# Kernel optimization log

Hardware: AMD Instinct MI355X
Metric: run time of the kernel (lower is better)

## Reference

```python
import jax, jax.numpy as jnp
import numpy as np

Na, Np, F, C, H, L, OUT = 50000, 100000, 128, 128, 8, 2, 64
D = C // H  # head dim = 16
E = 150000


def setup_inputs() -> dict:
    key = jax.random.key(0)
    ks = jax.random.split(key, 16)
    p = lambda k, shape: jax.random.normal(k, shape, jnp.float32) * 0.05
    return {
        "x_author": jax.random.normal(ks[0], (Na, F), jnp.float32),
        "x_paper": jax.random.normal(ks[1], (Np, F), jnp.float32),
        # per-node-type input projections (HGT.lin_dict)
        "win_w": p(ks[2], (2, F, C)), "win_b": p(ks[3], (2, C)),
        # per-layer, per-node-type K/Q/V linears of HGTConv
        "kqv_w": p(ks[4], (L, 2, 3, C, C)), "kqv_b": p(ks[5], (L, 2, 3, C)),
        # per-layer, per-node-type output linear a_lin
        "a_w": p(ks[6], (L, 2, C, C)), "a_b": p(ks[7], (L, 2, C)),
        # per-layer, per-node-type skip gate (init 1 like PyG)
        "skip": jnp.ones((L, 2), jnp.float32),
        # per-layer, per-edge-type relation matrices a_rel/m_rel and prior p_rel
        "rel_a": p(ks[8], (L, 2, H, D, D)), "rel_m": p(ks[9], (L, 2, H, D, D)),
        "rel_p": jnp.ones((L, 2, H), jnp.float32),
        # final classifier on author nodes
        "out_w": p(ks[10], (C, OUT)), "out_b": p(ks[11], (OUT,)),
        # edge type 0: author -> paper ('writes'); edge type 1: paper -> author (reverse)
        "ei_writes_src": jax.random.randint(ks[12], (E,), 0, Na, jnp.int32),
        "ei_writes_dst": jax.random.randint(ks[13], (E,), 0, Np, jnp.int32),
        "ei_rev_src": jax.random.randint(ks[14], (E,), 0, Np, jnp.int32),
        "ei_rev_dst": jax.random.randint(ks[15], (E,), 0, Na, jnp.int32),
    }


def _segment_softmax(alpha, dst, n):
    # softmax of alpha [E, H] over edges grouped by destination node (PyG softmax)
    m = jnp.full((n, alpha.shape[1]), -jnp.inf, alpha.dtype).at[dst].max(alpha)
    ex = jnp.exp(alpha - m[dst])
    s = jnp.zeros((n, alpha.shape[1]), alpha.dtype).at[dst].add(ex)
    return ex / (s[dst] + 1e-16)


def _hgt_forward(x_author, x_paper, win_w, win_b, kqv_w, kqv_b, a_w, a_b,
                 skip, rel_a, rel_m, rel_p, out_w, out_b, ei):
    # per-node-type input linear + relu
    xs = [jax.nn.relu(x_author @ win_w[0] + win_b[0]),
          jax.nn.relu(x_paper @ win_w[1] + win_b[1])]
    edge_types = [(0, 1, ei[0], ei[1]),  # author -> paper
                  (1, 0, ei[2], ei[3])]  # paper -> author
    nl = kqv_w.shape[0]
    inv_sqrt_d = np.float32(1.0 / np.sqrt(D))
    for l in range(nl):
        # K/Q/V per node type, shape [N_t, H, D]
        kqv = [[(xs[t] @ kqv_w[l, t, i] + kqv_b[l, t, i]).reshape(-1, H, D)
                for i in range(3)] for t in range(2)]
        agg = [jnp.zeros((xs[t].shape[0], H, D), xs[t].dtype) for t in range(2)]
        for e, (st, dt, src, dst) in enumerate(edge_types):
            # relation-specific transforms at node level, then gather at edges
            kn = jnp.einsum('nhd,hde->nhe', kqv[st][0], rel_a[l, e])
            vn = jnp.einsum('nhd,hde->nhe', kqv[st][2], rel_m[l, e])
            alpha = jnp.einsum('ehd,ehd->eh', kqv[dt][1][dst], kn[src])
            alpha = alpha * rel_p[l, e] * inv_sqrt_d
            alpha = _segment_softmax(alpha, dst, xs[dt].shape[0])
            agg[dt] = agg[dt].at[dst].add(alpha[:, :, None] * vn[src])
        new_xs = []
        for t in range(2):
            o = jax.nn.gelu(agg[t].reshape(-1, C), approximate=False)
            o = o @ a_w[l, t] + a_b[l, t]
            g = jax.nn.sigmoid(skip[l, t])
            new_xs.append(g * o + (1.0 - g) * xs[t])  # skip connection (dims match)
        xs = new_xs
    return xs[0] @ out_w + out_b  # author output


def reference(x_author, x_paper, win_w, win_b, kqv_w, kqv_b, a_w, a_b, skip,
              rel_a, rel_m, rel_p, out_w, out_b,
              ei_writes_src, ei_writes_dst, ei_rev_src, ei_rev_dst):
    ei = (ei_writes_src, ei_writes_dst, ei_rev_src, ei_rev_dst)
    return _hgt_forward(x_author, x_paper, win_w, win_b, kqv_w, kqv_b,
                        a_w, a_b, skip, rel_a, rel_m, rel_p, out_w, out_b, ei)
```

## Files before the change

kernel.cpp:

```cpp
#include <hip/hip_runtime.h>
#include <math.h>

namespace {

constexpr int Na = 50000, Np = 100000, L = 2, E = 150000;
constexpr int SCAN_TILE = 2048;

typedef __attribute__((ext_vector_type(8))) short short8v;
typedef __attribute__((ext_vector_type(4))) float f32x4;

__device__ inline float geluf(float x){ return 0.5f*x*(1.0f + erff(x*0.7071067811865476f)); }

__device__ inline float bf2f(unsigned short u){ return __uint_as_float(((unsigned)u) << 16); }
__device__ inline unsigned short f2bf(float f){
  unsigned u = __float_as_uint(f);
  u += 0x7FFFu + ((u >> 16) & 1u);
  return (unsigned short)(u >> 16);
}
__device__ inline unsigned pk2(float a, float b){
  return (unsigned)f2bf(a) | ((unsigned)f2bf(b) << 16);
}

struct StF32 {
  using T = float;
  static __device__ short8v ld8(const T* __restrict__ p){
    float4 lo = *reinterpret_cast<const float4*>(p);
    float4 hi = *reinterpret_cast<const float4*>(p+4);
    short8v v;
    v[0]=(short)f2bf(lo.x); v[1]=(short)f2bf(lo.y); v[2]=(short)f2bf(lo.z); v[3]=(short)f2bf(lo.w);
    v[4]=(short)f2bf(hi.x); v[5]=(short)f2bf(hi.y); v[6]=(short)f2bf(hi.z); v[7]=(short)f2bf(hi.w);
    return v;
  }
};
struct StBF16 {
  using T = unsigned short;
  static __device__ short8v ld8(const T* __restrict__ p){
    return *reinterpret_cast<const short8v*>(p);
  }
  static __device__ void ld16(const T* __restrict__ p, float* o){
    const uint4* q = reinterpret_cast<const uint4*>(p);
    #pragma unroll
    for (int half = 0; half < 2; ++half){
      uint4 u = q[half];
      o[half*8+0] = bf2f((unsigned short)(u.x & 0xffff));
      o[half*8+1] = bf2f((unsigned short)(u.x >> 16));
      o[half*8+2] = bf2f((unsigned short)(u.y & 0xffff));
      o[half*8+3] = bf2f((unsigned short)(u.y >> 16));
      o[half*8+4] = bf2f((unsigned short)(u.z & 0xffff));
      o[half*8+5] = bf2f((unsigned short)(u.z >> 16));
      o[half*8+6] = bf2f((unsigned short)(u.w & 0xffff));
      o[half*8+7] = bf2f((unsigned short)(u.w >> 16));
    }
  }
};

__global__ void zero_int_kernel(int* __restrict__ p, int n){
  int i = blockIdx.x*256 + threadIdx.x;
  int stride = gridDim.x*256;
  for (; i < n; i += stride) p[i] = 0;
}

__global__ void diag_kernel(float* o, float v){
  if (threadIdx.x == 0 && blockIdx.x == 0) o[0] = v;
}

__global__ void hist_kernel(const int* __restrict__ dst, int* __restrict__ counts, int nE){
  int e = blockIdx.x*256 + threadIdx.x;
  if (e >= nE) return;
  atomicAdd(&counts[dst[e]], 1);
}

__global__ void scan_a(const int* __restrict__ counts, int* __restrict__ bsum, int n){
  int base = blockIdx.x*SCAN_TILE;
  int s = 0;
  for (int i = threadIdx.x; i < SCAN_TILE; i += 256){
    int g = base + i;
    s += (g < n) ? counts[g] : 0;
  }
  __shared__ int red[256];
  red[threadIdx.x] = s;
  __syncthreads();
  for (int off = 128; off > 0; off >>= 1){
    if (threadIdx.x < off) red[threadIdx.x] += red[threadIdx.x + off];
    __syncthreads();
  }
  if (threadIdx.x == 0) bsum[blockIdx.x] = red[0];
}

__global__ void scan_b(int* __restrict__ bsum, int nb){
  __shared__ int sh[1024];
  int t = threadIdx.x;
  int v = (t < nb) ? bsum[t] : 0;
  sh[t] = v;
  __syncthreads();
  for (int off = 1; off < 1024; off <<= 1){
    int add = (t >= off) ? sh[t-off] : 0;
    __syncthreads();
    sh[t] += add;
    __syncthreads();
  }
  if (t < nb) bsum[t] = sh[t] - v;
}

__global__ void scan_c(int* __restrict__ counts, const int* __restrict__ bsum,
                       int* __restrict__ rp, int n){
  int base = blockIdx.x*SCAN_TILE;
  __shared__ int sh[SCAN_TILE];
  for (int i = threadIdx.x; i < SCAN_TILE; i += 256){
    int g = base + i;
    sh[i] = (g < n) ? counts[g] : 0;
  }
  __syncthreads();
  int t = threadIdx.x;
  int loc[8], s = 0;
  #pragma unroll
  for (int i = 0; i < 8; ++i){ loc[i] = s; s += sh[t*8 + i]; }
  __shared__ int red[256];
  red[t] = s;
  __syncthreads();
  for (int off = 1; off < 256; off <<= 1){
    int add = (t >= off) ? red[t-off] : 0;
    __syncthreads();
    red[t] += add;
    __syncthreads();
  }
  int texcl = red[t] - s + bsum[blockIdx.x];
  #pragma unroll
  for (int i = 0; i < 8; ++i){
    int g = base + t*8 + i;
    if (g < n){
      int v = texcl + loc[i];
      rp[g] = v;
      counts[g] = v;
      if (g == n-1) rp[n] = v + sh[t*8 + i];
    }
  }
}

__global__ void fill_slots_kernel(const int* __restrict__ src, const int* __restrict__ dst,
                                  int* __restrict__ cursor, int* __restrict__ slots, int nE){
  int e = blockIdx.x*256 + threadIdx.x;
  if (e >= nE) return;
  int slot = atomicAdd(&cursor[dst[e]], 1);
  slots[slot] = src[e];
}

__global__ void eff_w_kernel(const float* __restrict__ kqv_w, const float* __restrict__ kqv_b,
                             const float* __restrict__ rel_a, const float* __restrict__ rel_m,
                             float* __restrict__ effw, float* __restrict__ effb){
  int idx = blockIdx.x*256 + threadIdx.x;
  if (idx >= 2*2*2*128*128) return;
  int j = idx & 127; int f = (idx >> 7) & 127; int c = idx >> 14;
  int kv = c & 1, t = (c >> 1) & 1, l = c >> 2;
  int h = j >> 4, e2 = j & 15;
  int i = (kv == 0) ? 0 : 2;
  const float* W = kqv_w + ((size_t)(((l*2 + t)*3 + i)*128) + f)*128 + h*16;
  const float* A = ((kv == 0) ? rel_a : rel_m) + ((size_t)(l*2 + t)*8 + h)*256;
  float acc = 0.f;
  #pragma unroll
  for (int d = 0; d < 16; ++d) acc += W[d]*A[d*16 + e2];
  effw[(size_t)c*16384 + f*128 + j] = acc;
  if (f == 0){
    const float* B = kqv_b + (size_t)((l*2 + t)*3 + i)*128 + h*16;
    float ab = 0.f;
    #pragma unroll
    for (int d = 0; d < 16; ++d) ab += B[d]*A[d*16 + e2];
    effb[c*128 + j] = ab;
  }
}

struct PrepSrc { const float* s[19]; };
__global__ void prep_w_kernel(PrepSrc P, unsigned short* __restrict__ wbf){
  int idx = blockIdx.x*256 + threadIdx.x;
  if (idx >= 19*16384) return;
  int s = idx >> 14, j = idx & 16383;
  int n = j >> 7, k = j & 127;
  int nc = (s == 18) ? 64 : 128;
  if (n >= nc) return;
  wbf[(size_t)s*16384 + n*128 + k] = f2bf(P.s[s][(size_t)k*nc + n]);
}

__device__ inline void stage_w(short* Bs, const unsigned short* __restrict__ WT, int t, int rows){
  for (int c = t; c < rows*16; c += 512){
    int r = c >> 4, c16 = c & 15;
    short8v v = *reinterpret_cast<const short8v*>(&WT[r*128 + c16*8]);
    *reinterpret_cast<short8v*>(&Bs[r*128 + ((c16 ^ (r&7))<<3)]) = v;
  }
}

struct GemmArgs {
  const void* X[2];
  const unsigned short* WT[2];
  const float* bias[2];
  void* Y[2];
  const unsigned short* skip_x[2];
  const float* skip_s[2];
  int N[2];
  int blocks0;
};

template<int BN, int GELU_IN, int RELU_OUT, int SKIP, typename SIn>
__global__ __launch_bounds__(512) void gemm_kernel(GemmArgs Ar)
{
  __shared__ __align__(16) short As[128*128];
  __shared__ __align__(16) char Braw[32768];
  short* Bs = (short*)Braw;
  const int t = threadIdx.x;
  const int part = (blockIdx.x < Ar.blocks0) ? 0 : 1;
  const int bid = part ? (blockIdx.x - Ar.blocks0) : blockIdx.x;
  const typename SIn::T* X = (const typename SIn::T*)Ar.X[part];
  const unsigned short* WT = Ar.WT[part];
  const float* bias = Ar.bias[part];
  const int N = Ar.N[part];
  const int row0 = bid*128;
  for (int c = t; c < 128*16; c += 512){
    int r = c >> 4, c16 = c & 15;
    int gr = row0 + r;
    short8v v;
    if (gr < N){
      v = SIn::ld8(&X[(size_t)gr*128 + c16*8]);
      if (GELU_IN){
        #pragma unroll
        for (int i = 0; i < 8; ++i){
          float f = geluf(bf2f((unsigned short)v[i]));
          v[i] = (short)f2bf(f);
        }
      }
    } else {
      v = (short8v)0;
    }
    *reinterpret_cast<short8v*>(&As[r*128 + ((c16 ^ (r&7))<<3)]) = v;
  }
  stage_w(Bs, WT, t, BN);
  __syncthreads();
  const int lane = t & 63, wid = t >> 6;
  const int wm = wid >> 2, wn = wid & 3;
  constexpr int NR = BN/64;
  const int lr = lane & 15, lk = lane >> 4;
  f32x4 acc[4][NR] = {};
  #pragma unroll
  for (int kk = 0; kk < 4; ++kk){
    int kc = kk*4 + lk;
    short8v a[4], b[NR];
    #pragma unroll
    for (int m = 0; m < 4; ++m){
      int r = wm*64 + m*16 + lr;
      a[m] = *reinterpret_cast<const short8v*>(&As[r*128 + ((kc ^ (r&7))<<3)]);
    }
    #pragma unroll
    for (int n = 0; n < NR; ++n){
      int col = wn*(BN/4) + n*16 + lr;
      b[n] = *reinterpret_cast<const short8v*>(&Bs[col*128 + ((kc ^ (col&7))<<3)]);
    }
    #pragma unroll
    for (int m = 0; m < 4; ++m)
      #pragma unroll
      for (int n = 0; n < NR; ++n)
        acc[m][n] = __builtin_amdgcn_mfma_f32_16x16x32_bf16(b[n], a[m], acc[m][n], 0, 0, 0);
  }
  __syncthreads();

  if constexpr (BN == 128){
    #pragma unroll
    for (int m = 0; m < 4; ++m){
      int row = wm*64 + m*16 + lr;
      #pragma unroll
      for (int n = 0; n < NR; ++n){
        int col0 = wn*32 + n*16 + lk*4;
        float4 b4 = *reinterpret_cast<const float4*>(&bias[col0]);
        float y0 = acc[m][n][0] + b4.x, y1 = acc[m][n][1] + b4.y;
        float y2 = acc[m][n][2] + b4.z, y3 = acc[m][n][3] + b4.w;
        if (RELU_OUT){
          y0 = fmaxf(y0,0.f); y1 = fmaxf(y1,0.f); y2 = fmaxf(y2,0.f); y3 = fmaxf(y3,0.f);
        }
        uint2 pk; pk.x = pk2(y0,y1); pk.y = pk2(y2,y3);
        int c16 = col0 >> 3;
        *reinterpret_cast<uint2*>(&Bs[row*128 + ((c16 ^ (row&7))<<3) + (col0&7)]) = pk;
      }
    }
    __syncthreads();
    float g = 1.f, og = 0.f;
    if (SKIP){ float sv = *Ar.skip_s[part]; g = 1.f/(1.f + expf(-sv)); og = 1.f - g; }
    unsigned short* out = (unsigned short*)Ar.Y[part];
    const unsigned short* skip_x = Ar.skip_x[part];
    for (int c = t; c < 128*16; c += 512){
      int r = c >> 4, c16 = c & 15;
      int gr = row0 + r;
      if (gr >= N) continue;
      short8v v = *reinterpret_cast<const short8v*>(&Bs[r*128 + ((c16 ^ (r&7))<<3)]);
      if (SKIP){
        short8v s8 = *reinterpret_cast<const short8v*>(&skip_x[(size_t)gr*128 + c16*8]);
        short8v o8;
        #pragma unroll
        for (int i = 0; i < 8; ++i)
          o8[i] = (short)f2bf(g*bf2f((unsigned short)v[i]) + og*bf2f((unsigned short)s8[i]));
        *reinterpret_cast<short8v*>(&out[(size_t)gr*128 + c16*8]) = o8;
      } else {
        *reinterpret_cast<short8v*>(&out[(size_t)gr*128 + c16*8]) = v;
      }
    }
  } else {
    float* Bf = (float*)Braw;
    #pragma unroll
    for (int m = 0; m < 4; ++m){
      int row = wm*64 + m*16 + lr;
      #pragma unroll
      for (int n = 0; n < NR; ++n){
        int col0 = wn*16 + n*16 + lk*4;
        float4 b4 = *reinterpret_cast<const float4*>(&bias[col0]);
        float4 y;
        y.x = acc[m][n][0] + b4.x; y.y = acc[m][n][1] + b4.y;
        y.z = acc[m][n][2] + b4.z; y.w = acc[m][n][3] + b4.w;
        int cf = col0 >> 2;
        *reinterpret_cast<float4*>(&Bf[row*64 + ((cf ^ (row&7))<<2)]) = y;
      }
    }
    __syncthreads();
    float* out = (float*)Ar.Y[part];
    for (int c = t; c < 128*16; c += 512){
      int r = c >> 4, cf = c & 15;
      int gr = row0 + r;
      if (gr >= N) continue;
      float4 v = *reinterpret_cast<const float4*>(&Bf[r*64 + ((cf ^ (r&7))<<2)]);
      *reinterpret_cast<float4*>(&out[(size_t)gr*64 + cf*4]) = v;
    }
  }
}

struct QkvArgs {
  const unsigned short* X[2];
  const unsigned short* WT[2][3];
  const float* bias[2][3];
  unsigned short* out[2][3];
  int N[2];
  int blocks0;
};

__global__ __launch_bounds__(512) void qkv_kernel(QkvArgs Ar)
{
  __shared__ __align__(16) short As[128*128];
  __shared__ __align__(16) short Bs[128*128];
  const int t = threadIdx.x;
  const int part = (blockIdx.x < Ar.blocks0) ? 0 : 1;
  const int bid = part ? (blockIdx.x - Ar.blocks0) : blockIdx.x;
  const unsigned short* X = Ar.X[part];
  const int N = Ar.N[part];
  const int row0 = bid*128;
  for (int c = t; c < 128*16; c += 512){
    int r = c >> 4, c16 = c & 15;
    int gr = row0 + r;
    short8v v = (gr < N) ? *reinterpret_cast<const short8v*>(&X[(size_t)gr*128 + c16*8])
                         : (short8v)0;
    *reinterpret_cast<short8v*>(&As[r*128 + ((c16 ^ (r&7))<<3)]) = v;
  }
  const int lane = t & 63, wid = t >> 6;
  const int wm = wid >> 2, wn = wid & 3;
  const int lr = lane & 15, lk = lane >> 4;
  #pragma unroll
  for (int s = 0; s < 3; ++s){
    __syncthreads();
    stage_w(Bs, Ar.WT[part][s], t, 128);
    __syncthreads();
    f32x4 acc[4][2] = {};
    #pragma unroll
    for (int kk = 0; kk < 4; ++kk){
      int kc = kk*4 + lk;
      short8v a[4], b[2];
      #pragma unroll
      for (int m = 0; m < 4; ++m){
        int r = wm*64 + m*16 + lr;
        a[m] = *reinterpret_cast<const short8v*>(&As[r*128 + ((kc ^ (r&7))<<3)]);
      }
      #pragma unroll
      for (int n = 0; n < 2; ++n){
        int col = wn*32 + n*16 + lr;
        b[n] = *reinterpret_cast<const short8v*>(&Bs[col*128 + ((kc ^ (col&7))<<3)]);
      }
      #pragma unroll
      for (int m = 0; m < 4; ++m)
        #pragma unroll
        for (int n = 0; n < 2; ++n)
          acc[m][n] = __builtin_amdgcn_mfma_f32_16x16x32_bf16(b[n], a[m], acc[m][n], 0, 0, 0);
    }
    __syncthreads();
    const float* bi = Ar.bias[part][s];
    #pragma unroll
    for (int m = 0; m < 4; ++m){
      int row = wm*64 + m*16 + lr;
      #pragma unroll
      for (int n = 0; n < 2; ++n){
        int col0 = wn*32 + n*16 + lk*4;
        float4 b4 = *reinterpret_cast<const float4*>(&bi[col0]);
        uint2 pk;
        pk.x = pk2(acc[m][n][0] + b4.x, acc[m][n][1] + b4.y);
        pk.y = pk2(acc[m][n][2] + b4.z, acc[m][n][3] + b4.w);
        int c16 = col0 >> 3;
        *reinterpret_cast<uint2*>(&Bs[row*128 + ((c16 ^ (row&7))<<3) + (col0&7)]) = pk;
      }
    }
    __syncthreads();
    unsigned short* out = Ar.out[part][s];
    for (int c = t; c < 128*16; c += 512){
      int r = c >> 4, c16 = c & 15;
      int gr = row0 + r;
      if (gr >= N) continue;
      short8v v = *reinterpret_cast<const short8v*>(&Bs[r*128 + ((c16 ^ (r&7))<<3)]);
      *reinterpret_cast<short8v*>(&out[(size_t)gr*128 + c16*8]) = v;
    }
  }
}

struct AttnArgs {
  unsigned short* QA[2];
  const unsigned short* K[2];
  const unsigned short* V[2];
  const int* rp[2];
  const int* slots[2];
  const float* relp[2];
  int N[2];
  int blocks0;
};

__global__ void attn_gather_kernel(AttnArgs Ar){
  const int part = (blockIdx.x < Ar.blocks0) ? 0 : 1;
  const int bid = part ? (blockIdx.x - Ar.blocks0) : blockIdx.x;
  int idx = bid*256 + threadIdx.x;
  const int N = Ar.N[part];
  if (idx >= N*8) return;
  int h = idx & 7, n = idx >> 3;
  unsigned short* QA = Ar.QA[part];
  const unsigned short* K = Ar.K[part];
  const unsigned short* V = Ar.V[part];
  float q[16];
  StBF16::ld16(&QA[(size_t)n*128 + h*16], q);
  float scale_h = Ar.relp[part][h]*0.25f;
  float m = -INFINITY, s = 0.f, acc[16];
  #pragma unroll
  for (int i = 0; i < 16; ++i) acc[i] = 0.f;
  int b = Ar.rp[part][n], e = Ar.rp[part][n+1];
  const int* slots = Ar.slots[part];
  for (int j = b; j < e; ++j){
    int sv = slots[j];
    float kf[16], vf[16];
    StBF16::ld16(&K[(size_t)sv*128 + h*16], kf);
    float a = 0.f;
    #pragma unroll
    for (int i = 0; i < 16; ++i) a += q[i]*kf[i];
    a *= scale_h;
    float mn = fmaxf(m, a);
    float c = expf(m - mn);
    float p = expf(a - mn);
    StBF16::ld16(&V[(size_t)sv*128 + h*16], vf);
    s = s*c + p;
    #pragma unroll
    for (int i = 0; i < 16; ++i) acc[i] = acc[i]*c + p*vf[i];
    m = mn;
  }
  float inv = 1.f/(s + 1e-16f);
  #pragma unroll
  for (int i = 0; i < 16; ++i) QA[(size_t)n*128 + h*16 + i] = f2bf(acc[i]*inv);
}

struct Ptrs {
  const float *x_author, *x_paper, *win_w, *win_b, *kqv_w, *kqv_b, *a_w, *a_b;
  const float *skip, *rel_a, *rel_m, *rel_p, *out_w, *out_b;
  const int *src0, *dst0, *src1, *dst1;
};

static void run_pipeline(const Ptrs& P, float* d_out, char* ws, hipStream_t stream){
  using BF = unsigned short;
  size_t off = 0;
  auto alloc = [&](size_t bytes) -> void* {
    void* p = ws + off;
    off += (bytes + 255) & ~(size_t)255;
    return p;
  };
  BF* X0 = (BF*)alloc((size_t)Na*128*2);
  BF* X1 = (BF*)alloc((size_t)Np*128*2);
  BF* Q0 = (BF*)alloc((size_t)Na*128*2);
  BF* Q1 = (BF*)alloc((size_t)Np*128*2);
  BF* K0 = (BF*)alloc((size_t)Na*128*2);
  BF* K1 = (BF*)alloc((size_t)Np*128*2);
  BF* V0 = (BF*)alloc((size_t)Na*128*2);
  BF* V1 = (BF*)alloc((size_t)Np*128*2);
  float* effw = (float*)alloc((size_t)8*16384*4);
  float* effb = (float*)alloc((size_t)8*128*4);
  BF* wbf = (BF*)alloc((size_t)19*16384*2);
  int* rp0   = (int*)alloc((size_t)(Np+1)*4);
  int* cur0  = (int*)alloc((size_t)Np*4);
  int* slot0 = (int*)alloc((size_t)E*4);
  int* rp1   = (int*)alloc((size_t)(Na+1)*4);
  int* cur1  = (int*)alloc((size_t)Na*4);
  int* slot1 = (int*)alloc((size_t)E*4);
  int* bsum  = (int*)alloc((size_t)1024*4);

  auto cdiv = [](int a, int b){ return (a+b-1)/b; };
  const int geE = cdiv(E, 256);
  const int ga = cdiv(Na, 128), gp = cdiv(Np, 128);
  const int sb0 = cdiv(Np, SCAN_TILE), sb1 = cdiv(Na, SCAN_TILE);

  eff_w_kernel<<<512, 256, 0, stream>>>(P.kqv_w, P.kqv_b, P.rel_a, P.rel_m, effw, effb);

  PrepSrc ps;
  ps.s[0] = P.win_w; ps.s[1] = P.win_w + 16384;
  for (int l = 0; l < 2; ++l)
    for (int t = 0; t < 2; ++t){
      ps.s[2 + l*2 + t]  = P.kqv_w + (size_t)((l*2+t)*3+1)*16384;
      ps.s[6 + l*2 + t]  = effw + (size_t)(l*4+t*2+0)*16384;
      ps.s[10 + l*2 + t] = effw + (size_t)(l*4+t*2+1)*16384;
      ps.s[14 + l*2 + t] = P.a_w + (size_t)(l*2+t)*16384;
    }
  ps.s[18] = P.out_w;
  prep_w_kernel<<<cdiv(19*16384,256),256,0,stream>>>(ps, wbf);

  zero_int_kernel<<<512,256,0,stream>>>(cur0, Np);
  zero_int_kernel<<<512,256,0,stream>>>(cur1, Na);
  hist_kernel<<<geE,256,0,stream>>>(P.dst0, cur0, E);
  hist_kernel<<<geE,256,0,stream>>>(P.dst1, cur1, E);
  scan_a<<<sb0,256,0,stream>>>(cur0, bsum, Np);
  scan_b<<<1,1024,0,stream>>>(bsum, sb0);
  scan_c<<<sb0,256,0,stream>>>(cur0, bsum, rp0, Np);
  scan_a<<<sb1,256,0,stream>>>(cur1, bsum, Na);
  scan_b<<<1,1024,0,stream>>>(bsum, sb1);
  scan_c<<<sb1,256,0,stream>>>(cur1, bsum, rp1, Na);
  fill_slots_kernel<<<geE,256,0,stream>>>(P.src0, P.dst0, cur0, slot0, E);
  fill_slots_kernel<<<geE,256,0,stream>>>(P.src1, P.dst1, cur1, slot1, E);

  auto W = [&](int s){ return wbf + (size_t)s*16384; };

  {
    GemmArgs g{};
    g.X[0] = P.x_author; g.X[1] = P.x_paper;
    g.WT[0] = W(0); g.WT[1] = W(1);
    g.bias[0] = P.win_b; g.bias[1] = P.win_b + 128;
    g.Y[0] = X0; g.Y[1] = X1;
    g.N[0] = Na; g.N[1] = Np; g.blocks0 = ga;
    gemm_kernel<128,0,1,0,StF32><<<ga+gp,512,0,stream>>>(g);
  }

  const int ab0 = cdiv(Np*8,256), ab1 = cdiv(Na*8,256);

  for (int l = 0; l < L; ++l){
    QkvArgs q{};
    q.X[0] = X0; q.X[1] = X1;
    for (int t2 = 0; t2 < 2; ++t2){
      q.WT[t2][0] = W(2+l*2+t2); q.WT[t2][1] = W(6+l*2+t2); q.WT[t2][2] = W(10+l*2+t2);
      q.bias[t2][0] = P.kqv_b + ((l*2+t2)*3+1)*128;
      q.bias[t2][1] = effb + (l*4+t2*2+0)*128;
      q.bias[t2][2] = effb + (l*4+t2*2+1)*128;
    }
    q.out[0][0] = Q0; q.out[0][1] = K0; q.out[0][2] = V0;
    q.out[1][0] = Q1; q.out[1][1] = K1; q.out[1][2] = V1;
    q.N[0] = Na; q.N[1] = Np; q.blocks0 = ga;
    qkv_kernel<<<ga+gp,512,0,stream>>>(q);

    AttnArgs a{};
    a.QA[0] = Q1; a.K[0] = K0; a.V[0] = V0; a.rp[0] = rp0; a.slots[0] = slot0;
    a.relp[0] = P.rel_p + (l*2+0)*8; a.N[0] = Np;
    a.QA[1] = Q0; a.K[1] = K1; a.V[1] = V1; a.rp[1] = rp1; a.slots[1] = slot1;
    a.relp[1] = P.rel_p + (l*2+1)*8; a.N[1] = Na;
    a.blocks0 = ab0;
    attn_gather_kernel<<<ab0+ab1,256,0,stream>>>(a);

    GemmArgs g{};
    g.X[0] = Q0; g.X[1] = Q1;
    g.WT[0] = W(14+l*2+0); g.WT[1] = W(14+l*2+1);
    g.bias[0] = P.a_b + (l*2+0)*128; g.bias[1] = P.a_b + (l*2+1)*128;
    g.Y[0] = X0; g.Y[1] = X1;
    g.skip_x[0] = X0; g.skip_x[1] = X1;
    g.skip_s[0] = P.skip + (l*2+0); g.skip_s[1] = P.skip + (l*2+1);
    g.N[0] = Na; g.N[1] = Np; g.blocks0 = ga;
    gemm_kernel<128,1,0,1,StBF16><<<ga+gp,512,0,stream>>>(g);
  }

  {
    GemmArgs g{};
    g.X[0] = X0; g.X[1] = nullptr;
    g.WT[0] = W(18); g.WT[1] = nullptr;
    g.bias[0] = P.out_b; g.bias[1] = nullptr;
    g.Y[0] = d_out; g.Y[1] = nullptr;
    g.N[0] = Na; g.N[1] = 0; g.blocks0 = ga;
    gemm_kernel<64,0,0,0,StBF16><<<ga,512,0,stream>>>(g);
  }
}

static size_t plan_bytes(){
  auto al = [](size_t x){ return (x + 255) & ~(size_t)255; };
  size_t t = 0;
  t += 4*(al((size_t)Na*128*2) + al((size_t)Np*128*2));
  t += al((size_t)8*16384*4) + al((size_t)8*128*4) + al((size_t)19*16384*2);
  t += al((size_t)(Np+1)*4) + al((size_t)Np*4) + al((size_t)E*4);
  t += al((size_t)(Na+1)*4) + al((size_t)Na*4) + al((size_t)E*4);
  t += al((size_t)1024*4);
  return t;
}

}

extern "C" void kernel_launch(void* const* d_in, const int* in_sizes, int n_in,
                              void* d_out, int out_size, void* d_ws, size_t ws_size,
                              hipStream_t stream){
  Ptrs P;
  P.x_author = (const float*)d_in[0];
  P.x_paper  = (const float*)d_in[1];
  P.win_w = (const float*)d_in[2];
  P.win_b = (const float*)d_in[3];
  P.kqv_w = (const float*)d_in[4];
  P.kqv_b = (const float*)d_in[5];
  P.a_w   = (const float*)d_in[6];
  P.a_b   = (const float*)d_in[7];
  P.skip  = (const float*)d_in[8];
  P.rel_a = (const float*)d_in[9];
  P.rel_m = (const float*)d_in[10];
  P.rel_p = (const float*)d_in[11];
  P.out_w = (const float*)d_in[12];
  P.out_b = (const float*)d_in[13];
  P.src0 = (const int*)d_in[14];
  P.dst0 = (const int*)d_in[15];
  P.src1 = (const int*)d_in[16];
  P.dst1 = (const int*)d_in[17];

  if (ws_size >= plan_bytes()){
    run_pipeline(P, (float*)d_out, (char*)d_ws, stream);
  } else {
    diag_kernel<<<1,1,0,stream>>>((float*)d_out, (float)((double)ws_size/1.0e6));
  }
}
```

Baseline: 336.0 us.

## Use 1024-thread GEMM blocks, separate result LDS, prefetch weights, fuse GELU into attention

Doubles GEMM and QKV block size so each wave computes 32 rows instead of 64, adding a dedicated LDS result buffer so the post-MFMA barrier can be dropped. In the QKV kernel the next weight matrix is staged into LDS while the current result is written out. GELU is moved from the a_lin GEMM input load into the attention output store. The larger LDS footprint and smaller per-wave tiles may reduce occupancy or MFMA reuse.

Result: slower. 379.3 us (+12.9%).

```diff
diff --git a/kernel.cpp b/kernel.cpp
--- a/kernel.cpp
+++ b/kernel.cpp
@@ -180,8 +180,9 @@
   wbf[(size_t)s*16384 + n*128 + k] = f2bf(P.s[s][(size_t)k*nc + n]);
 }
 
+template<int NT>
 __device__ inline void stage_w(short* Bs, const unsigned short* __restrict__ WT, int t, int rows){
-  for (int c = t; c < rows*16; c += 512){
+  for (int c = t; c < rows*16; c += NT){
     int r = c >> 4, c16 = c & 15;
     short8v v = *reinterpret_cast<const short8v*>(&WT[r*128 + c16*8]);
     *reinterpret_cast<short8v*>(&Bs[r*128 + ((c16 ^ (r&7))<<3)]) = v;
@@ -199,12 +200,13 @@
   int blocks0;
 };
 
-template<int BN, int GELU_IN, int RELU_OUT, int SKIP, typename SIn>
-__global__ __launch_bounds__(512) void gemm_kernel(GemmArgs Ar)
+template<int BN, int RELU_OUT, int SKIP, typename SIn>
+__global__ __launch_bounds__(1024) void gemm_kernel(GemmArgs Ar)
 {
   __shared__ __align__(16) short As[128*128];
-  __shared__ __align__(16) char Braw[32768];
-  short* Bs = (short*)Braw;
+  __shared__ __align__(16) short Bs[BN*128];
+  __shared__ __align__(16) char Rraw[32768];
+  short* Rs = (short*)Rraw;
   const int t = threadIdx.x;
   const int part = (blockIdx.x < Ar.blocks0) ? 0 : 1;
   const int bid = part ? (blockIdx.x - Ar.blocks0) : blockIdx.x;
@@ -213,38 +215,26 @@
   const float* bias = Ar.bias[part];
   const int N = Ar.N[part];
   const int row0 = bid*128;
-  for (int c = t; c < 128*16; c += 512){
+  for (int c = t; c < 2048; c += 1024){
     int r = c >> 4, c16 = c & 15;
     int gr = row0 + r;
-    short8v v;
-    if (gr < N){
-      v = SIn::ld8(&X[(size_t)gr*128 + c16*8]);
-      if (GELU_IN){
-        #pragma unroll
-        for (int i = 0; i < 8; ++i){
-          float f = geluf(bf2f((unsigned short)v[i]));
-          v[i] = (short)f2bf(f);
-        }
-      }
-    } else {
-      v = (short8v)0;
-    }
+    short8v v = (gr < N) ? SIn::ld8(&X[(size_t)gr*128 + c16*8]) : (short8v)0;
     *reinterpret_cast<short8v*>(&As[r*128 + ((c16 ^ (r&7))<<3)]) = v;
   }
-  stage_w(Bs, WT, t, BN);
+  stage_w<1024>(Bs, WT, t, BN);
   __syncthreads();
   const int lane = t & 63, wid = t >> 6;
   const int wm = wid >> 2, wn = wid & 3;
   constexpr int NR = BN/64;
   const int lr = lane & 15, lk = lane >> 4;
-  f32x4 acc[4][NR] = {};
+  f32x4 acc[2][NR] = {};
   #pragma unroll
   for (int kk = 0; kk < 4; ++kk){
     int kc = kk*4 + lk;
-    short8v a[4], b[NR];
-    #pragma unroll
-    for (int m = 0; m < 4; ++m){
-      int r = wm*64 + m*16 + lr;
+    short8v a[2], b[NR];
+    #pragma unroll
+    for (int m = 0; m < 2; ++m){
+      int r = wm*32 + m*16 + lr;
       a[m] = *reinterpret_cast<const short8v*>(&As[r*128 + ((kc ^ (r&7))<<3)]);
     }
     #pragma unroll
@@ -253,17 +243,16 @@
       b[n] = *reinterpret_cast<const short8v*>(&Bs[col*128 + ((kc ^ (col&7))<<3)]);
     }
     #pragma unroll
-    for (int m = 0; m < 4; ++m)
+    for (int m = 0; m < 2; ++m)
       #pragma unroll
       for (int n = 0; n < NR; ++n)
         acc[m][n] = __builtin_amdgcn_mfma_f32_16x16x32_bf16(b[n], a[m], acc[m][n], 0, 0, 0);
   }
-  __syncthreads();
 
   if constexpr (BN == 128){
     #pragma unroll
-    for (int m = 0; m < 4; ++m){
-      int row = wm*64 + m*16 + lr;
+    for (int m = 0; m < 2; ++m){
+      int row = wm*32 + m*16 + lr;
       #pragma unroll
       for (int n = 0; n < NR; ++n){
         int col0 = wn*32 + n*16 + lk*4;
@@ -275,7 +264,7 @@
         }
         uint2 pk; pk.x = pk2(y0,y1); pk.y = pk2(y2,y3);
         int c16 = col0 >> 3;
-        *reinterpret_cast<uint2*>(&Bs[row*128 + ((c16 ^ (row&7))<<3) + (col0&7)]) = pk;
+        *reinterpret_cast<uint2*>(&Rs[row*128 + ((c16 ^ (row&7))<<3) + (col0&7)]) = pk;
       }
     }
     __syncthreads();
@@ -283,11 +272,11 @@
     if (SKIP){ float sv = *Ar.skip_s[part]; g = 1.f/(1.f + expf(-sv)); og = 1.f - g; }
     unsigned short* out = (unsigned short*)Ar.Y[part];
     const unsigned short* skip_x = Ar.skip_x[part];
-    for (int c = t; c < 128*16; c += 512){
+    for (int c = t; c < 2048; c += 1024){
       int r = c >> 4, c16 = c & 15;
       int gr = row0 + r;
       if (gr >= N) continue;
-      short8v v = *reinterpret_cast<const short8v*>(&Bs[r*128 + ((c16 ^ (r&7))<<3)]);
+      short8v v = *reinterpret_cast<const short8v*>(&Rs[r*128 + ((c16 ^ (r&7))<<3)]);
       if (SKIP){
         short8v s8 = *reinterpret_cast<const short8v*>(&skip_x[(size_t)gr*128 + c16*8]);
         short8v o8;
@@ -300,28 +289,25 @@
       }
     }
   } else {
-    float* Bf = (float*)Braw;
-    #pragma unroll
-    for (int m = 0; m < 4; ++m){
-      int row = wm*64 + m*16 + lr;
-      #pragma unroll
-      for (int n = 0; n < NR; ++n){
-        int col0 = wn*16 + n*16 + lk*4;
-        float4 b4 = *reinterpret_cast<const float4*>(&bias[col0]);
-        float4 y;
-        y.x = acc[m][n][0] + b4.x; y.y = acc[m][n][1] + b4.y;
-        y.z = acc[m][n][2] + b4.z; y.w = acc[m][n][3] + b4.w;
-        int cf = col0 >> 2;
-        *reinterpret_cast<float4*>(&Bf[row*64 + ((cf ^ (row&7))<<2)]) = y;
-      }
+    float* Rf = (float*)Rraw;
+    #pragma unroll
+    for (int m = 0; m < 2; ++m){
+      int row = wm*32 + m*16 + lr;
+      int col0 = wn*16 + lk*4;
+      float4 b4 = *reinterpret_cast<const float4*>(&bias[col0]);
+      float4 y;
+      y.x = acc[m][0][0] + b4.x; y.y = acc[m][0][1] + b4.y;
+      y.z = acc[m][0][2] + b4.z; y.w = acc[m][0][3] + b4.w;
+      int cf = col0 >> 2;
+      *reinterpret_cast<float4*>(&Rf[row*64 + ((cf ^ (row&7))<<2)]) = y;
     }
     __syncthreads();
     float* out = (float*)Ar.Y[part];
-    for (int c = t; c < 128*16; c += 512){
+    for (int c = t; c < 2048; c += 1024){
       int r = c >> 4, cf = c & 15;
       int gr = row0 + r;
       if (gr >= N) continue;
-      float4 v = *reinterpret_cast<const float4*>(&Bf[r*64 + ((cf ^ (r&7))<<2)]);
+      float4 v = *reinterpret_cast<const float4*>(&Rf[r*64 + ((cf ^ (r&7))<<2)]);
       *reinterpret_cast<float4*>(&out[(size_t)gr*64 + cf*4]) = v;
     }
   }
@@ -336,39 +322,39 @@
   int blocks0;
 };
 
-__global__ __launch_bounds__(512) void qkv_kernel(QkvArgs Ar)
+__global__ __launch_bounds__(1024) void qkv_kernel(QkvArgs Ar)
 {
   __shared__ __align__(16) short As[128*128];
   __shared__ __align__(16) short Bs[128*128];
+  __shared__ __align__(16) short Rs[128*128];
   const int t = threadIdx.x;
   const int part = (blockIdx.x < Ar.blocks0) ? 0 : 1;
   const int bid = part ? (blockIdx.x - Ar.blocks0) : blockIdx.x;
   const unsigned short* X = Ar.X[part];
   const int N = Ar.N[part];
   const int row0 = bid*128;
-  for (int c = t; c < 128*16; c += 512){
+  for (int c = t; c < 2048; c += 1024){
     int r = c >> 4, c16 = c & 15;
     int gr = row0 + r;
     short8v v = (gr < N) ? *reinterpret_cast<const short8v*>(&X[(size_t)gr*128 + c16*8])
                          : (short8v)0;
     *reinterpret_cast<short8v*>(&As[r*128 + ((c16 ^ (r&7))<<3)]) = v;
   }
+  stage_w<1024>(Bs, Ar.WT[part][0], t, 128);
+  __syncthreads();
   const int lane = t & 63, wid = t >> 6;
   const int wm = wid >> 2, wn = wid & 3;
   const int lr = lane & 15, lk = lane >> 4;
   #pragma unroll
   for (int s = 0; s < 3; ++s){
-    __syncthreads();
-    stage_w(Bs, Ar.WT[part][s], t, 128);
-    __syncthreads();
-    f32x4 acc[4][2] = {};
+    f32x4 acc[2][2] = {};
     #pragma unroll
     for (int kk = 0; kk < 4; ++kk){
       int kc = kk*4 + lk;
-      short8v a[4], b[2];
+      short8v a[2], b[2];
       #pragma unroll
-      for (int m = 0; m < 4; ++m){
-        int r = wm*64 + m*16 + lr;
+      for (int m = 0; m < 2; ++m){
+        int r = wm*32 + m*16 + lr;
         a[m] = *reinterpret_cast<const short8v*>(&As[r*128 + ((kc ^ (r&7))<<3)]);
       }
       #pragma unroll
@@ -377,16 +363,15 @@
         b[n] = *reinterpret_cast<const short8v*>(&Bs[col*128 + ((kc ^ (col&7))<<3)]);
       }
       #pragma unroll
-      for (int m = 0; m < 4; ++m)
+      for (int m = 0; m < 2; ++m)
         #pragma unroll
         for (int n = 0; n < 2; ++n)
           acc[m][n] = __builtin_amdgcn_mfma_f32_16x16x32_bf16(b[n], a[m], acc[m][n], 0, 0, 0);
     }
-    __syncthreads();
     const float* bi = Ar.bias[part][s];
     #pragma unroll
-    for (int m = 0; m < 4; ++m){
-      int row = wm*64 + m*16 + lr;
+    for (int m = 0; m < 2; ++m){
+      int row = wm*32 + m*16 + lr;
       #pragma unroll
       for (int n = 0; n < 2; ++n){
         int col0 = wn*32 + n*16 + lk*4;
@@ -395,18 +380,20 @@
         pk.x = pk2(acc[m][n][0] + b4.x, acc[m][n][1] + b4.y);
         pk.y = pk2(acc[m][n][2] + b4.z, acc[m][n][3] + b4.w);
         int c16 = col0 >> 3;
-        *reinterpret_cast<uint2*>(&Bs[row*128 + ((c16 ^ (row&7))<<3) + (col0&7)]) = pk;
+        *reinterpret_cast<uint2*>(&Rs[row*128 + ((c16 ^ (row&7))<<3) + (col0&7)]) = pk;
       }
     }
     __syncthreads();
+    if (s < 2) stage_w<1024>(Bs, Ar.WT[part][s+1], t, 128);
     unsigned short* out = Ar.out[part][s];
-    for (int c = t; c < 128*16; c += 512){
+    for (int c = t; c < 2048; c += 1024){
       int r = c >> 4, c16 = c & 15;
       int gr = row0 + r;
       if (gr >= N) continue;
-      short8v v = *reinterpret_cast<const short8v*>(&Bs[r*128 + ((c16 ^ (r&7))<<3)]);
+      short8v v = *reinterpret_cast<const short8v*>(&Rs[r*128 + ((c16 ^ (r&7))<<3)]);
       *reinterpret_cast<short8v*>(&out[(size_t)gr*128 + c16*8]) = v;
     }
+    __syncthreads();
   }
 }
 
@@ -458,7 +445,8 @@
   }
   float inv = 1.f/(s + 1e-16f);
   #pragma unroll
-  for (int i = 0; i < 16; ++i) QA[(size_t)n*128 + h*16 + i] = f2bf(acc[i]*inv);
+  for (int i = 0; i < 16; ++i)
+    QA[(size_t)n*128 + h*16 + i] = f2bf(geluf(acc[i]*inv));
 }
 
 struct Ptrs {
@@ -535,7 +523,7 @@
     g.bias[0] = P.win_b; g.bias[1] = P.win_b + 128;
     g.Y[0] = X0; g.Y[1] = X1;
     g.N[0] = Na; g.N[1] = Np; g.blocks0 = ga;
-    gemm_kernel<128,0,1,0,StF32><<<ga+gp,512,0,stream>>>(g);
+    gemm_kernel<128,1,0,StF32><<<ga+gp,1024,0,stream>>>(g);
   }
 
   const int ab0 = cdiv(Np*8,256), ab1 = cdiv(Na*8,256);
@@ -552,7 +540,7 @@
     q.out[0][0] = Q0; q.out[0][1] = K0; q.out[0][2] = V0;
     q.out[1][0] = Q1; q.out[1][1] = K1; q.out[1][2] = V1;
     q.N[0] = Na; q.N[1] = Np; q.blocks0 = ga;
-    qkv_kernel<<<ga+gp,512,0,stream>>>(q);
+    qkv_kernel<<<ga+gp,1024,0,stream>>>(q);
 
     AttnArgs a{};
     a.QA[0] = Q1; a.K[0] = K0; a.V[0] = V0; a.rp[0] = rp0; a.slots[0] = slot0;
@@ -570,7 +558,7 @@
     g.skip_x[0] = X0; g.skip_x[1] = X1;
     g.skip_s[0] = P.skip + (l*2+0); g.skip_s[1] = P.skip + (l*2+1);
     g.N[0] = Na; g.N[1] = Np; g.blocks0 = ga;
-    gemm_kernel<128,1,0,1,StBF16><<<ga+gp,512,0,stream>>>(g);
+    gemm_kernel<128,0,1,StBF16><<<ga+gp,1024,0,stream>>>(g);
   }
 
   {
@@ -580,7 +568,7 @@
     g.bias[0] = P.out_b; g.bias[1] = nullptr;
     g.Y[0] = d_out; g.Y[1] = nullptr;
     g.N[0] = Na; g.N[1] = 0; g.blocks0 = ga;
-    gemm_kernel<64,0,0,0,StBF16><<<ga,512,0,stream>>>(g);
+    gemm_kernel<64,0,0,StBF16><<<ga,1024,0,stream>>>(g);
   }
 }
 
```

## Interleave K and V per head, unroll attention gather, fuse GELU into attention

Applied to the files above, without the earlier changes.

The QKV kernel now writes K and V into one interleaved buffer, so each head's 16 K values and 16 V values sit next to each other (64 contiguous bytes per source node and head). The attention gather reads both with one pointer and processes two edges per iteration, which raises memory-level parallelism for the random gathers. GELU moves from the GEMM's A-tile load into the attention epilogue, so it is computed once per output element rather than inside the GEMM staging. The risks are more registers in the unrolled loop and a changed write pattern in the QKV store.

Result: slower. 388.1 us (+15.5%).

```diff
diff --git a/kernel.cpp b/kernel.cpp
--- a/kernel.cpp
+++ b/kernel.cpp
@@ -199,7 +199,7 @@
   int blocks0;
 };
 
-template<int BN, int GELU_IN, int RELU_OUT, int SKIP, typename SIn>
+template<int BN, int RELU_OUT, int SKIP, typename SIn>
 __global__ __launch_bounds__(512) void gemm_kernel(GemmArgs Ar)
 {
   __shared__ __align__(16) short As[128*128];
@@ -213,22 +213,10 @@
   const float* bias = Ar.bias[part];
   const int N = Ar.N[part];
   const int row0 = bid*128;
-  for (int c = t; c < 128*16; c += 512){
+  for (int c = t; c < 2048; c += 512){
     int r = c >> 4, c16 = c & 15;
     int gr = row0 + r;
-    short8v v;
-    if (gr < N){
-      v = SIn::ld8(&X[(size_t)gr*128 + c16*8]);
-      if (GELU_IN){
-        #pragma unroll
-        for (int i = 0; i < 8; ++i){
-          float f = geluf(bf2f((unsigned short)v[i]));
-          v[i] = (short)f2bf(f);
-        }
-      }
-    } else {
-      v = (short8v)0;
-    }
+    short8v v = (gr < N) ? SIn::ld8(&X[(size_t)gr*128 + c16*8]) : (short8v)0;
     *reinterpret_cast<short8v*>(&As[r*128 + ((c16 ^ (r&7))<<3)]) = v;
   }
   stage_w(Bs, WT, t, BN);
@@ -283,7 +271,7 @@
     if (SKIP){ float sv = *Ar.skip_s[part]; g = 1.f/(1.f + expf(-sv)); og = 1.f - g; }
     unsigned short* out = (unsigned short*)Ar.Y[part];
     const unsigned short* skip_x = Ar.skip_x[part];
-    for (int c = t; c < 128*16; c += 512){
+    for (int c = t; c < 2048; c += 512){
       int r = c >> 4, c16 = c & 15;
       int gr = row0 + r;
       if (gr >= N) continue;
@@ -304,20 +292,17 @@
     #pragma unroll
     for (int m = 0; m < 4; ++m){
       int row = wm*64 + m*16 + lr;
-      #pragma unroll
-      for (int n = 0; n < NR; ++n){
-        int col0 = wn*16 + n*16 + lk*4;
-        float4 b4 = *reinterpret_cast<const float4*>(&bias[col0]);
-        float4 y;
-        y.x = acc[m][n][0] + b4.x; y.y = acc[m][n][1] + b4.y;
-        y.z = acc[m][n][2] + b4.z; y.w = acc[m][n][3] + b4.w;
-        int cf = col0 >> 2;
-        *reinterpret_cast<float4*>(&Bf[row*64 + ((cf ^ (row&7))<<2)]) = y;
-      }
+      int col0 = wn*16 + lk*4;
+      float4 b4 = *reinterpret_cast<const float4*>(&bias[col0]);
+      float4 y;
+      y.x = acc[m][0][0] + b4.x; y.y = acc[m][0][1] + b4.y;
+      y.z = acc[m][0][2] + b4.z; y.w = acc[m][0][3] + b4.w;
+      int cf = col0 >> 2;
+      *reinterpret_cast<float4*>(&Bf[row*64 + ((cf ^ (row&7))<<2)]) = y;
     }
     __syncthreads();
     float* out = (float*)Ar.Y[part];
-    for (int c = t; c < 128*16; c += 512){
+    for (int c = t; c < 2048; c += 512){
       int r = c >> 4, cf = c & 15;
       int gr = row0 + r;
       if (gr >= N) continue;
@@ -346,7 +331,7 @@
   const unsigned short* X = Ar.X[part];
   const int N = Ar.N[part];
   const int row0 = bid*128;
-  for (int c = t; c < 128*16; c += 512){
+  for (int c = t; c < 2048; c += 512){
     int r = c >> 4, c16 = c & 15;
     int gr = row0 + r;
     short8v v = (gr < N) ? *reinterpret_cast<const short8v*>(&X[(size_t)gr*128 + c16*8])
@@ -400,20 +385,24 @@
     }
     __syncthreads();
     unsigned short* out = Ar.out[part][s];
-    for (int c = t; c < 128*16; c += 512){
+    for (int c = t; c < 2048; c += 512){
       int r = c >> 4, c16 = c & 15;
       int gr = row0 + r;
       if (gr >= N) continue;
       short8v v = *reinterpret_cast<const short8v*>(&Bs[r*128 + ((c16 ^ (r&7))<<3)]);
-      *reinterpret_cast<short8v*>(&out[(size_t)gr*128 + c16*8]) = v;
+      if (s == 0){
+        *reinterpret_cast<short8v*>(&out[(size_t)gr*128 + c16*8]) = v;
+      } else {
+        int kc16 = ((c16 >> 1) << 2) | (c16 & 1) | ((s == 2) ? 2 : 0);
+        *reinterpret_cast<short8v*>(&out[(size_t)gr*256 + kc16*8]) = v;
+      }
     }
   }
 }
 
 struct AttnArgs {
   unsigned short* QA[2];
-  const unsigned short* K[2];
-  const unsigned short* V[2];
+  const unsigned short* KV[2];
   const int* rp[2];
   const int* slots[2];
   const float* relp[2];
@@ -429,8 +418,7 @@
   if (idx >= N*8) return;
   int h = idx & 7, n = idx >> 3;
   unsigned short* QA = Ar.QA[part];
-  const unsigned short* K = Ar.K[part];
-  const unsigned short* V = Ar.V[part];
+  const unsigned short* KV = Ar.KV[part];
   float q[16];
   StBF16::ld16(&QA[(size_t)n*128 + h*16], q);
   float scale_h = Ar.relp[part][h]*0.25f;
@@ -439,18 +427,42 @@
   for (int i = 0; i < 16; ++i) acc[i] = 0.f;
   int b = Ar.rp[part][n], e = Ar.rp[part][n+1];
   const int* slots = Ar.slots[part];
-  for (int j = b; j < e; ++j){
+  int j = b;
+  for (; j + 2 <= e; j += 2){
+    int sv0 = slots[j], sv1 = slots[j+1];
+    const unsigned short* p0 = KV + (size_t)sv0*256 + h*32;
+    const unsigned short* p1 = KV + (size_t)sv1*256 + h*32;
+    float kf0[16], vf0[16], kf1[16], vf1[16];
+    StBF16::ld16(p0, kf0); StBF16::ld16(p0+16, vf0);
+    StBF16::ld16(p1, kf1); StBF16::ld16(p1+16, vf1);
+    float a0 = 0.f, a1 = 0.f;
+    #pragma unroll
+    for (int i = 0; i < 16; ++i){ a0 += q[i]*kf0[i]; a1 += q[i]*kf1[i]; }
+    a0 *= scale_h; a1 *= scale_h;
+    float mn = fmaxf(m, a0);
+    float c = expf(m - mn), p = expf(a0 - mn);
+    s = s*c + p;
+    #pragma unroll
+    for (int i = 0; i < 16; ++i) acc[i] = acc[i]*c + p*vf0[i];
+    m = mn;
+    mn = fmaxf(m, a1);
+    c = expf(m - mn); p = expf(a1 - mn);
+    s = s*c + p;
+    #pragma unroll
+    for (int i = 0; i < 16; ++i) acc[i] = acc[i]*c + p*vf1[i];
+    m = mn;
+  }
+  if (j < e){
     int sv = slots[j];
+    const unsigned short* p0 = KV + (size_t)sv*256 + h*32;
     float kf[16], vf[16];
-    StBF16::ld16(&K[(size_t)sv*128 + h*16], kf);
+    StBF16::ld16(p0, kf); StBF16::ld16(p0+16, vf);
     float a = 0.f;
     #pragma unroll
     for (int i = 0; i < 16; ++i) a += q[i]*kf[i];
     a *= scale_h;
     float mn = fmaxf(m, a);
-    float c = expf(m - mn);
-    float p = expf(a - mn);
-    StBF16::ld16(&V[(size_t)sv*128 + h*16], vf);
+    float c = expf(m - mn), p = expf(a - mn);
     s = s*c + p;
     #pragma unroll
     for (int i = 0; i < 16; ++i) acc[i] = acc[i]*c + p*vf[i];
@@ -458,7 +470,8 @@
   }
   float inv = 1.f/(s + 1e-16f);
   #pragma unroll
-  for (int i = 0; i < 16; ++i) QA[(size_t)n*128 + h*16 + i] = f2bf(acc[i]*inv);
+  for (int i = 0; i < 16; ++i)
+    QA[(size_t)n*128 + h*16 + i] = f2bf(geluf(acc[i]*inv));
 }
 
 struct Ptrs {
@@ -479,10 +492,8 @@
   BF* X1 = (BF*)alloc((size_t)Np*128*2);
   BF* Q0 = (BF*)alloc((size_t)Na*128*2);
   BF* Q1 = (BF*)alloc((size_t)Np*128*2);
-  BF* K0 = (BF*)alloc((size_t)Na*128*2);
-  BF* K1 = (BF*)alloc((size_t)Np*128*2);
-  BF* V0 = (BF*)alloc((size_t)Na*128*2);
-  BF* V1 = (BF*)alloc((size_t)Np*128*2);
+  BF* KV0 = (BF*)alloc((size_t)Na*256*2);
+  BF* KV1 = (BF*)alloc((size_t)Np*256*2);
   float* effw = (float*)alloc((size_t)8*16384*4);
   float* effb = (float*)alloc((size_t)8*128*4);
   BF* wbf = (BF*)alloc((size_t)19*16384*2);
@@ -535,7 +546,7 @@
     g.bias[0] = P.win_b; g.bias[1] = P.win_b + 128;
     g.Y[0] = X0; g.Y[1] = X1;
     g.N[0] = Na; g.N[1] = Np; g.blocks0 = ga;
-    gemm_kernel<128,0,1,0,StF32><<<ga+gp,512,0,stream>>>(g);
+    gemm_kernel<128,1,0,StF32><<<ga+gp,512,0,stream>>>(g);
   }
 
   const int ab0 = cdiv(Np*8,256), ab1 = cdiv(Na*8,256);
@@ -549,15 +560,15 @@
       q.bias[t2][1] = effb + (l*4+t2*2+0)*128;
       q.bias[t2][2] = effb + (l*4+t2*2+1)*128;
     }
-    q.out[0][0] = Q0; q.out[0][1] = K0; q.out[0][2] = V0;
-    q.out[1][0] = Q1; q.out[1][1] = K1; q.out[1][2] = V1;
+    q.out[0][0] = Q0; q.out[0][1] = KV0; q.out[0][2] = KV0;
+    q.out[1][0] = Q1; q.out[1][1] = KV1; q.out[1][2] = KV1;
     q.N[0] = Na; q.N[1] = Np; q.blocks0 = ga;
     qkv_kernel<<<ga+gp,512,0,stream>>>(q);
 
     AttnArgs a{};
-    a.QA[0] = Q1; a.K[0] = K0; a.V[0] = V0; a.rp[0] = rp0; a.slots[0] = slot0;
+    a.QA[0] = Q1; a.KV[0] = KV0; a.rp[0] = rp0; a.slots[0] = slot0;
     a.relp[0] = P.rel_p + (l*2+0)*8; a.N[0] = Np;
-    a.QA[1] = Q0; a.K[1] = K1; a.V[1] = V1; a.rp[1] = rp1; a.slots[1] = slot1;
+    a.QA[1] = Q0; a.KV[1] = KV1; a.rp[1] = rp1; a.slots[1] = slot1;
     a.relp[1] = P.rel_p + (l*2+1)*8; a.N[1] = Na;
     a.blocks0 = ab0;
     attn_gather_kernel<<<ab0+ab1,256,0,stream>>>(a);
@@ -570,7 +581,7 @@
     g.skip_x[0] = X0; g.skip_x[1] = X1;
     g.skip_s[0] = P.skip + (l*2+0); g.skip_s[1] = P.skip + (l*2+1);
     g.N[0] = Na; g.N[1] = Np; g.blocks0 = ga;
-    gemm_kernel<128,1,0,1,StBF16><<<ga+gp,512,0,stream>>>(g);
+    gemm_kernel<128,0,1,StBF16><<<ga+gp,512,0,stream>>>(g);
   }
 
   {
@@ -580,14 +591,15 @@
     g.bias[0] = P.out_b; g.bias[1] = nullptr;
     g.Y[0] = d_out; g.Y[1] = nullptr;
     g.N[0] = Na; g.N[1] = 0; g.blocks0 = ga;
-    gemm_kernel<64,0,0,0,StBF16><<<ga,512,0,stream>>>(g);
+    gemm_kernel<64,0,0,StBF16><<<ga,512,0,stream>>>(g);
   }
 }
 
 static size_t plan_bytes(){
   auto al = [](size_t x){ return (x + 255) & ~(size_t)255; };
   size_t t = 0;
-  t += 4*(al((size_t)Na*128*2) + al((size_t)Np*128*2));
+  t += 2*(al((size_t)Na*128*2) + al((size_t)Np*128*2));
+  t += al((size_t)Na*256*2) + al((size_t)Np*256*2);
   t += al((size_t)8*16384*4) + al((size_t)8*128*4) + al((size_t)19*16384*2);
   t += al((size_t)(Np+1)*4) + al((size_t)Np*4) + al((size_t)E*4);
   t += al((size_t)(Na+1)*4) + al((size_t)Na*4) + al((size_t)E*4);
```
